# Kernel optimization log

Measured on AMD Instinct MI355X. Metric: run time of the kernel, lower is better.

Reference implementation:

```python
import jax, jax.numpy as jnp
import numpy as np

EMBED_DIM = 1024
NUM_HEADS = 16
D_K = EMBED_DIM // NUM_HEADS  # 64 quantum wires per head


def setup_inputs() -> dict:
    key = jax.random.key(0)
    k1, k2, k3 = jax.random.split(key, 3)
    x = jax.random.normal(k1, (8, 2048, EMBED_DIM), dtype=jnp.float32)
    # single shared projection weight (source creates ONE nn.Linear used for q,k,v and out)
    W = jax.random.normal(k2, (EMBED_DIM, EMBED_DIM), dtype=jnp.float32) * 0.02
    # trainable RY angles, one per wire, shared across tokens and heads
    theta = jax.random.normal(k3, (D_K,), dtype=jnp.float32)
    return {"x": x, "W": W, "theta": theta}


def _quantum_project(h, theta):
    # h: [B, S, E] -> per-head wires [B, S, H, d_k]
    # Circuit per wire i: |0> -> RX(h_i) -> RY(theta_i) -> <Z>
    # Product state closed form: <Z> = cos(theta_i) * cos(h_i)
    B, S, E = h.shape
    hw = h.reshape(B, S, NUM_HEADS, D_K)
    return jnp.cos(theta) * jnp.cos(hw)  # [B, S, H, d_k]


def reference(x, W, theta):
    # one Linear (no bias) shared by q, k, v -> identical projections
    proj = x @ W.T  # [B, S, E]
    qq = _quantum_project(proj, theta)  # == k_q == v_q, [B, S, H, d_k]
    # scores attend heads-vs-heads per token (faithful to source matmul on dims -2,-1)
    scores = jnp.einsum('bshd,bsgd->bshg', qq, qq) / np.sqrt(D_K).astype(np.float32)
    attn = jax.nn.softmax(scores, axis=-1)  # dropout omitted (eval)
    out = jnp.einsum('bshg,bsgd->bshd', attn, qq)  # [B, S, H, d_k]
    B, S = x.shape[0], x.shape[1]
    out = out.reshape(B, S, EMBED_DIM) @ W.T  # output projection with same shared linear
    return out
```

## Files before the change

### kernel.cpp

```cpp
#include <hip/hip_runtime.h>
#include <hip/hip_bf16.h>
#include <stdint.h>

#define NB    8
#define NS    2048
#define NE    1024
#define NH    16
#define NDK   64
#define MTOK  (NB*NS)

typedef __attribute__((ext_vector_type(8))) short bf16x8;
typedef __attribute__((ext_vector_type(4))) float f32x4;

__device__ __forceinline__ ushort f2bf(float f) {
  uint32_t u = __float_as_uint(f);
  u += 0x7FFFu + ((u >> 16) & 1u);
  return (ushort)(u >> 16);
}

__device__ __forceinline__ void gload16(const void* g, void* l) {
  __builtin_amdgcn_global_load_lds(
      (const __attribute__((address_space(1))) void*)g,
      (__attribute__((address_space(3))) void*)l, 16, 0, 0);
}

__global__ __launch_bounds__(256) void cvt_bf16(const float* __restrict__ in,
                                                ushort* __restrict__ out, int n4) {
  int stride = gridDim.x * blockDim.x;
  for (int j = blockIdx.x * blockDim.x + threadIdx.x; j < n4; j += stride) {
    float4 v = ((const float4*)in)[j];
    ushort4 o;
    o.x = f2bf(v.x); o.y = f2bf(v.y); o.z = f2bf(v.z); o.w = f2bf(v.w);
    ((ushort4*)out)[j] = o;
  }
}

#define GM 256
#define GN 256
#define GK 64

template<int EPI>
__global__ __launch_bounds__(512, 2) void gemm256(const ushort* __restrict__ A,
                                                  const ushort* __restrict__ Bm,
                                                  float* __restrict__ Cf,
                                                  ushort* __restrict__ Cq,
                                                  const float* __restrict__ theta,
                                                  int M, int N, int K) {
  __shared__ ushort As[2][GM * GK];
  __shared__ ushort Bs[2][GN * GK];

  const int tid  = threadIdx.x;
  const int wid  = tid >> 6;
  const int lane = tid & 63;
  const int wr   = wid >> 2;
  const int wc   = wid & 3;
  const int fr   = lane & 15;
  const int ks   = lane >> 4;

  int b  = blockIdx.x;
  int wg = ((b & 7) << 5) | (b >> 3);
  int br = wg >> 2, bc = wg & 3;

  const ushort* Abase = A  + (size_t)(br * GM) * K;
  const ushort* Bbase = Bm + (size_t)(bc * GN) * K;

  const int srow = lane >> 3;
  const int sch8 = ((lane & 7) ^ srow) * 8;

  const int sA0 = ((0 + ks) ^ (fr & 7)) * 8;
  const int sA1 = ((4 + ks) ^ (fr & 7)) * 8;

  f32x4 zero = {0.f, 0.f, 0.f, 0.f};
  f32x4 acc[8][4];
#pragma unroll
  for (int mi = 0; mi < 8; ++mi)
#pragma unroll
    for (int ni = 0; ni < 4; ++ni) acc[mi][ni] = zero;

  auto stA = [&](int buf, int mh, int kt) {
#pragma unroll
    for (int j = 0; j < 2; ++j) {
      int rl = mh * 128 + j * 64 + wid * 8;
      gload16(Abase + (size_t)(rl + srow) * K + kt * GK + sch8,
              &As[buf][rl * GK]);
    }
  };
  auto stB = [&](int buf, int mh, int kt) {
#pragma unroll
    for (int j = 0; j < 2; ++j) {
      int rl = mh * 128 + j * 64 + wid * 8;
      gload16(Bbase + (size_t)(rl + srow) * K + kt * GK + sch8,
              &Bs[buf][rl * GK]);
    }
  };

  stB(0, 0, 0); stB(0, 1, 0); stA(0, 0, 0); stA(0, 1, 0);
  asm volatile("s_waitcnt vmcnt(0)" ::: "memory");
  __builtin_amdgcn_s_barrier();

  const int NKT = K / GK;
  int cur = 0;
  for (int t = 0; t < NKT; ++t) {
    const ushort* Ac = As[cur];
    const ushort* Bc = Bs[cur];
    const int nb = cur ^ 1;
    const bool pf = (t + 1 < NKT);
    bf16x8 af[4], bv[4];

#pragma unroll
    for (int mi = 0; mi < 4; ++mi)
      af[mi] = *(const bf16x8*)&Ac[(mi * 32 + wr * 16 + fr) * GK + sA0];
#pragma unroll
    for (int ni = 0; ni < 4; ++ni)
      bv[ni] = *(const bf16x8*)&Bc[(ni * 64 + wc * 16 + fr) * GK + sA0];
    if (pf) stB(nb, 0, t + 1);
    __builtin_amdgcn_sched_barrier(0);
    __builtin_amdgcn_s_setprio(1);
#pragma unroll
    for (int mi = 0; mi < 4; ++mi)
#pragma unroll
      for (int ni = 0; ni < 4; ++ni)
        acc[mi][ni] = __builtin_amdgcn_mfma_f32_16x16x32_bf16(af[mi], bv[ni], acc[mi][ni], 0, 0, 0);
    __builtin_amdgcn_s_setprio(0);
    __builtin_amdgcn_sched_barrier(0);
    if (pf) asm volatile("s_waitcnt vmcnt(2)" ::: "memory");
    else    asm volatile("s_waitcnt vmcnt(0)" ::: "memory");
    __builtin_amdgcn_s_barrier();

#pragma unroll
    for (int mi = 0; mi < 4; ++mi)
      af[mi] = *(const bf16x8*)&Ac[((mi + 4) * 32 + wr * 16 + fr) * GK + sA0];
    if (pf) stB(nb, 1, t + 1);
    __builtin_amdgcn_sched_barrier(0);
    __builtin_amdgcn_s_setprio(1);
#pragma unroll
    for (int mi = 0; mi < 4; ++mi)
#pragma unroll
      for (int ni = 0; ni < 4; ++ni)
        acc[mi + 4][ni] = __builtin_amdgcn_mfma_f32_16x16x32_bf16(af[mi], bv[ni], acc[mi + 4][ni], 0, 0, 0);
    __builtin_amdgcn_s_setprio(0);
    __builtin_amdgcn_sched_barrier(0);
    __builtin_amdgcn_s_barrier();

#pragma unroll
    for (int mi = 0; mi < 4; ++mi)
      af[mi] = *(const bf16x8*)&Ac[(mi * 32 + wr * 16 + fr) * GK + sA1];
#pragma unroll
    for (int ni = 0; ni < 4; ++ni)
      bv[ni] = *(const bf16x8*)&Bc[(ni * 64 + wc * 16 + fr) * GK + sA1];
    if (pf) stA(nb, 0, t + 1);
    __builtin_amdgcn_sched_barrier(0);
    __builtin_amdgcn_s_setprio(1);
#pragma unroll
    for (int mi = 0; mi < 4; ++mi)
#pragma unroll
      for (int ni = 0; ni < 4; ++ni)
        acc[mi][ni] = __builtin_amdgcn_mfma_f32_16x16x32_bf16(af[mi], bv[ni], acc[mi][ni], 0, 0, 0);
    __builtin_amdgcn_s_setprio(0);
    __builtin_amdgcn_sched_barrier(0);
    __builtin_amdgcn_s_barrier();

#pragma unroll
    for (int mi = 0; mi < 4; ++mi)
      af[mi] = *(const bf16x8*)&Ac[((mi + 4) * 32 + wr * 16 + fr) * GK + sA1];
    if (pf) stA(nb, 1, t + 1);
    __builtin_amdgcn_sched_barrier(0);
    __builtin_amdgcn_s_setprio(1);
#pragma unroll
    for (int mi = 0; mi < 4; ++mi)
#pragma unroll
      for (int ni = 0; ni < 4; ++ni)
        acc[mi + 4][ni] = __builtin_amdgcn_mfma_f32_16x16x32_bf16(af[mi], bv[ni], acc[mi + 4][ni], 0, 0, 0);
    __builtin_amdgcn_s_setprio(0);
    __builtin_amdgcn_sched_barrier(0);
    if (pf) asm volatile("s_waitcnt vmcnt(2)" ::: "memory");
    __builtin_amdgcn_s_barrier();

    cur ^= 1;
  }

  const int colL = wc * 16 + fr;
  float ct = 0.f;
  if (EPI == 1) ct = __cosf(theta[colL]);
#pragma unroll
  for (int mi = 0; mi < 8; ++mi) {
    int row0 = br * GM + mi * 32 + wr * 16 + ks * 4;
#pragma unroll
    for (int ni = 0; ni < 4; ++ni) {
      size_t cbase = (size_t)row0 * N + bc * GN + ni * 64 + colL;
#pragma unroll
      for (int i = 0; i < 4; ++i) {
        if (EPI == 1)
          Cq[cbase + (size_t)i * N] = f2bf(ct * __cosf(acc[mi][ni][i]));
        else
          Cf[cbase + (size_t)i * N] = acc[mi][ni][i];
      }
    }
  }
}

__global__ __launch_bounds__(256) void attn_quantum(const ushort* __restrict__ qqb,
                                                    ushort* __restrict__ aout) {
  __shared__ ushort T[4][64 * 32];
  int tid = threadIdx.x;
  int wv  = tid >> 6, l = tid & 63;
  size_t tok = (size_t)blockIdx.x * 4 + wv;
  const ushort* src = qqb + tok * NE;
  ushort* Tw = T[wv];

  int h  = l & 15;
  int kb = l >> 4;

  bf16x8 f0 = *(const bf16x8*)(src + h * 64 + kb * 8);
  bf16x8 f1 = *(const bf16x8*)(src + h * 64 + kb * 8 + 32);

#pragma unroll
  for (int jj = 0; jj < 8; ++jj) {
    int d0 = kb * 8 + jj;
    int d1 = d0 + 32;
    Tw[d0 * 32 + (((h >> 3) ^ ((d0 >> 3) & 3)) << 3) + (h & 7)] = (ushort)f0[jj];
    Tw[d1 * 32 + (((h >> 3) ^ ((d1 >> 3) & 3)) << 3) + (h & 7)] = (ushort)f1[jj];
  }

  f32x4 sa = {0.f, 0.f, 0.f, 0.f};
  sa = __builtin_amdgcn_mfma_f32_16x16x32_bf16(f0, f0, sa, 0, 0, 0);
  sa = __builtin_amdgcn_mfma_f32_16x16x32_bf16(f1, f1, sa, 0, 0, 0);

  float s[4];
#pragma unroll
  for (int i = 0; i < 4; ++i) s[i] = sa[i] * 0.125f;

  float mx = fmaxf(fmaxf(s[0], s[1]), fmaxf(s[2], s[3]));
  mx = fmaxf(mx, __shfl_xor(mx, 16));
  mx = fmaxf(mx, __shfl_xor(mx, 32));
  float e[4], sum = 0.f;
#pragma unroll
  for (int i = 0; i < 4; ++i) { e[i] = __expf(s[i] - mx); sum += e[i]; }
  sum += __shfl_xor(sum, 16);
  sum += __shfl_xor(sum, 32);
  float inv = 1.f / sum;
#pragma unroll
  for (int i = 0; i < 4; ++i) e[i] *= inv;

  int s1 = h + (kb & 1) * 32;
  float q1[4], q2[4];
#pragma unroll
  for (int i = 0; i < 4; ++i) {
    q1[i] = __shfl(e[i], s1);
    q2[i] = __shfl(e[i], s1 + 16);
  }
  bool live = (kb < 2);
  bf16x8 pa;
#pragma unroll
  for (int i = 0; i < 4; ++i) {
    pa[i]     = live ? (short)f2bf(q1[i]) : (short)0;
    pa[4 + i] = live ? (short)f2bf(q2[i]) : (short)0;
  }

  __syncthreads();

  f32x4 o[4];
#pragma unroll
  for (int c = 0; c < 4; ++c) {
    int r = c * 16 + h;
    int slot = (kb & 1) ^ ((r >> 3) & 3);
    bf16x8 bfrag = *(const bf16x8*)&Tw[r * 32 + slot * 8];
    f32x4 z = {0.f, 0.f, 0.f, 0.f};
    o[c] = __builtin_amdgcn_mfma_f32_16x16x32_bf16(pa, bfrag, z, 0, 0, 0);
  }

  ushort* dst = aout + tok * NE;
#pragma unroll
  for (int c = 0; c < 4; ++c)
#pragma unroll
    for (int i = 0; i < 4; ++i)
      dst[(kb * 4 + i) * NDK + c * 16 + h] = f2bf(o[c][i]);
}

extern "C" void kernel_launch(void* const* d_in, const int* in_sizes, int n_in,
                              void* d_out, int out_size, void* d_ws, size_t ws_size,
                              hipStream_t stream) {
  const float* x     = (const float*)d_in[0];
  const float* W     = (const float*)d_in[1];
  const float* theta = (const float*)d_in[2];
  float* out = (float*)d_out;

  char* ws = (char*)d_ws;
  ushort* xb  = (ushort*)ws;
  ushort* Wb  = (ushort*)(ws + (size_t)MTOK * NE * 2);
  ushort* qqb = (ushort*)(ws + (size_t)MTOK * NE * 2 + (size_t)NE * NE * 2);
  ushort* aout = xb;

  cvt_bf16<<<1024, 256, 0, stream>>>(x, xb, MTOK * NE / 4);
  cvt_bf16<<<256, 256, 0, stream>>>(W, Wb, NE * NE / 4);

  int nwg = (MTOK / GM) * (NE / GN);
  gemm256<1><<<nwg, 512, 0, stream>>>(xb, Wb, nullptr, qqb, theta, MTOK, NE, NE);

  attn_quantum<<<MTOK / 4, 256, 0, stream>>>(qqb, aout);

  gemm256<0><<<nwg, 512, 0, stream>>>(aout, Wb, out, nullptr, nullptr, MTOK, NE, NE);
}
```

Measured before the change: 109.6 us.

## Fuse fp32-to-bf16 conversion of x into first GEMM's A-tile loads

Drops the separate pass that converts x from fp32 to bf16. The first GEMM now loads fp32 A tiles into registers, converts them and writes them into LDS at the end of each k-step. This removes a full read and write of the 64 MB activation tensor, but the first GEMM reads twice as many A bytes and adds register pressure and a synchronous conversion step before each barrier. The prefetch schedule for both GEMM modes also changes: all next-tile loads are issued at the start of each iteration, with adjusted wait counts.

```diff
diff --git a/kernel.cpp b/kernel.cpp
--- a/kernel.cpp
+++ b/kernel.cpp
@@ -39,8 +39,9 @@
 #define GN 256
 #define GK 64
 
-template<int EPI>
-__global__ __launch_bounds__(512, 2) void gemm256(const ushort* __restrict__ A,
+template<int MODE>
+__global__ __launch_bounds__(512, 2) void gemm256(const ushort* __restrict__ Ab,
+                                                  const float* __restrict__ Af,
                                                   const ushort* __restrict__ Bm,
                                                   float* __restrict__ Cf,
                                                   ushort* __restrict__ Cq,
@@ -61,14 +62,18 @@
   int wg = ((b & 7) << 5) | (b >> 3);
   int br = wg >> 2, bc = wg & 3;
 
-  const ushort* Abase = A  + (size_t)(br * GM) * K;
   const ushort* Bbase = Bm + (size_t)(bc * GN) * K;
+  const ushort* Abase = (MODE == 0) ? (Ab + (size_t)(br * GM) * K) : nullptr;
+  const float4* Af4   = (MODE == 1) ? ((const float4*)Af) : nullptr;
 
   const int srow = lane >> 3;
   const int sch8 = ((lane & 7) ^ srow) * 8;
 
   const int sA0 = ((0 + ks) ^ (fr & 7)) * 8;
   const int sA1 = ((4 + ks) ^ (fr & 7)) * 8;
+
+  const int cs    = lane & 7;
+  const int wslot = (cs ^ srow) * 8;
 
   f32x4 zero = {0.f, 0.f, 0.f, 0.f};
   f32x4 acc[8][4];
@@ -94,8 +99,39 @@
     }
   };
 
-  stB(0, 0, 0); stB(0, 1, 0); stA(0, 0, 0); stA(0, 1, 0);
-  asm volatile("s_waitcnt vmcnt(0)" ::: "memory");
+  float4 ar[8];
+  auto loadA = [&](int kt) {
+#pragma unroll
+    for (int j = 0; j < 4; ++j) {
+      int rl = wid * 32 + j * 8 + srow;
+      size_t base = (size_t)(br * GM + rl) * (K / 4) + kt * 16 + cs * 2;
+      ar[2 * j]     = Af4[base];
+      ar[2 * j + 1] = Af4[base + 1];
+    }
+  };
+  auto writeA = [&](int buf) {
+#pragma unroll
+    for (int j = 0; j < 4; ++j) {
+      int rl = wid * 32 + j * 8 + srow;
+      bf16x8 v;
+      v[0] = (short)f2bf(ar[2*j].x);   v[1] = (short)f2bf(ar[2*j].y);
+      v[2] = (short)f2bf(ar[2*j].z);   v[3] = (short)f2bf(ar[2*j].w);
+      v[4] = (short)f2bf(ar[2*j+1].x); v[5] = (short)f2bf(ar[2*j+1].y);
+      v[6] = (short)f2bf(ar[2*j+1].z); v[7] = (short)f2bf(ar[2*j+1].w);
+      *(bf16x8*)&As[buf][rl * GK + wslot] = v;
+    }
+  };
+
+  stB(0, 0, 0); stB(0, 1, 0);
+  if (MODE == 0) {
+    stA(0, 0, 0); stA(0, 1, 0);
+    asm volatile("s_waitcnt vmcnt(2)" ::: "memory");
+  } else {
+    loadA(0);
+    asm volatile("s_waitcnt vmcnt(0)" ::: "memory");
+    writeA(0);
+    asm volatile("s_waitcnt lgkmcnt(0)" ::: "memory");
+  }
   __builtin_amdgcn_s_barrier();
 
   const int NKT = K / GK;
@@ -113,7 +149,11 @@
 #pragma unroll
     for (int ni = 0; ni < 4; ++ni)
       bv[ni] = *(const bf16x8*)&Bc[(ni * 64 + wc * 16 + fr) * GK + sA0];
-    if (pf) stB(nb, 0, t + 1);
+    if (pf) {
+      stB(nb, 0, t + 1); stB(nb, 1, t + 1);
+      if (MODE == 0) { stA(nb, 0, t + 1); stA(nb, 1, t + 1); }
+      else           loadA(t + 1);
+    }
     __builtin_amdgcn_sched_barrier(0);
     __builtin_amdgcn_s_setprio(1);
 #pragma unroll
@@ -123,14 +163,15 @@
         acc[mi][ni] = __builtin_amdgcn_mfma_f32_16x16x32_bf16(af[mi], bv[ni], acc[mi][ni], 0, 0, 0);
     __builtin_amdgcn_s_setprio(0);
     __builtin_amdgcn_sched_barrier(0);
-    if (pf) asm volatile("s_waitcnt vmcnt(2)" ::: "memory");
-    else    asm volatile("s_waitcnt vmcnt(0)" ::: "memory");
+    if (MODE == 0) {
+      if (pf) asm volatile("s_waitcnt vmcnt(8)" ::: "memory");
+      else    asm volatile("s_waitcnt vmcnt(0)" ::: "memory");
+    }
     __builtin_amdgcn_s_barrier();
 
 #pragma unroll
     for (int mi = 0; mi < 4; ++mi)
       af[mi] = *(const bf16x8*)&Ac[((mi + 4) * 32 + wr * 16 + fr) * GK + sA0];
-    if (pf) stB(nb, 1, t + 1);
     __builtin_amdgcn_sched_barrier(0);
     __builtin_amdgcn_s_setprio(1);
 #pragma unroll
@@ -148,7 +189,6 @@
 #pragma unroll
     for (int ni = 0; ni < 4; ++ni)
       bv[ni] = *(const bf16x8*)&Bc[(ni * 64 + wc * 16 + fr) * GK + sA1];
-    if (pf) stA(nb, 0, t + 1);
     __builtin_amdgcn_sched_barrier(0);
     __builtin_amdgcn_s_setprio(1);
 #pragma unroll
@@ -163,7 +203,6 @@
 #pragma unroll
     for (int mi = 0; mi < 4; ++mi)
       af[mi] = *(const bf16x8*)&Ac[((mi + 4) * 32 + wr * 16 + fr) * GK + sA1];
-    if (pf) stA(nb, 1, t + 1);
     __builtin_amdgcn_sched_barrier(0);
     __builtin_amdgcn_s_setprio(1);
 #pragma unroll
@@ -173,7 +212,15 @@
         acc[mi + 4][ni] = __builtin_amdgcn_mfma_f32_16x16x32_bf16(af[mi], bv[ni], acc[mi + 4][ni], 0, 0, 0);
     __builtin_amdgcn_s_setprio(0);
     __builtin_amdgcn_sched_barrier(0);
-    if (pf) asm volatile("s_waitcnt vmcnt(2)" ::: "memory");
+    if (MODE == 0) {
+      if (pf) asm volatile("s_waitcnt vmcnt(2)" ::: "memory");
+    } else {
+      if (pf) {
+        asm volatile("s_waitcnt vmcnt(0)" ::: "memory");
+        writeA(nb);
+        asm volatile("s_waitcnt lgkmcnt(0)" ::: "memory");
+      }
+    }
     __builtin_amdgcn_s_barrier();
 
     cur ^= 1;
@@ -181,7 +228,7 @@
 
   const int colL = wc * 16 + fr;
   float ct = 0.f;
-  if (EPI == 1) ct = __cosf(theta[colL]);
+  if (MODE == 1) ct = __cosf(theta[colL]);
 #pragma unroll
   for (int mi = 0; mi < 8; ++mi) {
     int row0 = br * GM + mi * 32 + wr * 16 + ks * 4;
@@ -190,7 +237,7 @@
       size_t cbase = (size_t)row0 * N + bc * GN + ni * 64 + colL;
 #pragma unroll
       for (int i = 0; i < 4; ++i) {
-        if (EPI == 1)
+        if (MODE == 1)
           Cq[cbase + (size_t)i * N] = f2bf(ct * __cosf(acc[mi][ni][i]));
         else
           Cf[cbase + (size_t)i * N] = acc[mi][ni][i];
@@ -286,18 +333,16 @@
   float* out = (float*)d_out;
 
   char* ws = (char*)d_ws;
-  ushort* xb  = (ushort*)ws;
-  ushort* Wb  = (ushort*)(ws + (size_t)MTOK * NE * 2);
-  ushort* qqb = (ushort*)(ws + (size_t)MTOK * NE * 2 + (size_t)NE * NE * 2);
-  ushort* aout = xb;
-
-  cvt_bf16<<<1024, 256, 0, stream>>>(x, xb, MTOK * NE / 4);
+  ushort* Wb   = (ushort*)ws;
+  ushort* qqb  = (ushort*)(ws + (size_t)NE * NE * 2);
+  ushort* aout = (ushort*)(ws + (size_t)NE * NE * 2 + (size_t)MTOK * NE * 2);
+
   cvt_bf16<<<256, 256, 0, stream>>>(W, Wb, NE * NE / 4);
 
   int nwg = (MTOK / GM) * (NE / GN);
-  gemm256<1><<<nwg, 512, 0, stream>>>(xb, Wb, nullptr, qqb, theta, MTOK, NE, NE);
+  gemm256<1><<<nwg, 512, 0, stream>>>(nullptr, x, Wb, nullptr, qqb, theta, MTOK, NE, NE);
 
   attn_quantum<<<MTOK / 4, 256, 0, stream>>>(qqb, aout);
 
-  gemm256<0><<<nwg, 512, 0, stream>>>(aout, Wb, out, nullptr, nullptr, MTOK, NE, NE);
-}
+  gemm256<0><<<nwg, 512, 0, stream>>>(aout, nullptr, Wb, out, nullptr, nullptr, MTOK, NE, NE);
+}
```

Result: faster. 106.8 us (-2.6%).
